# Optimization experiments

Measured on AMD Instinct MI355X. Metric: run time of the kernel, lower is better.

Reference implementation:

```python
import jax, jax.numpy as jnp
import numpy as np

N_ACTIONS = 4
HIDDEN = 32

def setup_inputs() -> dict:
    key = jax.random.key(0)
    ks = jax.random.split(key, 8)
    B, T = 2048, 1024
    prev_actions_onehot = jax.random.uniform(ks[0], (B, T, N_ACTIONS), dtype=jnp.float32)
    prev_rewards = jax.random.normal(ks[1], (B, T, 1), dtype=jnp.float32)
    in_dim = N_ACTIONS + 1
    s_ih = 1.0 / np.sqrt(HIDDEN)
    W_ih = jax.random.uniform(ks[2], (HIDDEN, in_dim), jnp.float32, -s_ih, s_ih)
    W_hh = jax.random.uniform(ks[3], (HIDDEN, HIDDEN), jnp.float32, -s_ih, s_ih)
    b_ih = jax.random.uniform(ks[4], (HIDDEN,), jnp.float32, -s_ih, s_ih)
    b_hh = jax.random.uniform(ks[5], (HIDDEN,), jnp.float32, -s_ih, s_ih)
    W_ro = jax.random.uniform(ks[6], (N_ACTIONS, HIDDEN), jnp.float32, -s_ih, s_ih)
    b_ro = jax.random.uniform(ks[7], (N_ACTIONS,), jnp.float32, -s_ih, s_ih)
    return {
        'prev_actions_onehot': prev_actions_onehot,
        'prev_rewards': prev_rewards,
        'W_ih': W_ih, 'W_hh': W_hh, 'b_ih': b_ih, 'b_hh': b_hh,
        'W_ro': W_ro, 'b_ro': b_ro,
    }

def reference(prev_actions_onehot, prev_rewards, W_ih, W_hh, b_ih, b_hh, W_ro, b_ro):
    # x_seq: [B, T, n_actions+1]
    x_seq = jnp.concatenate([prev_actions_onehot, prev_rewards], axis=-1)
    B = x_seq.shape[0]
    # Precompute the input projection for all steps (parallel): [B, T, H]
    x_proj = jnp.einsum('bti,hi->bth', x_seq, W_ih) + b_ih + b_hh
    h0 = jnp.zeros((B, HIDDEN), dtype=x_seq.dtype)

    def step(h, xp_t):
        # xp_t: [B, H] (already contains x@W_ih^T + b_ih + b_hh)
        h_new = jnp.tanh(xp_t + h @ W_hh.T)
        return h_new, h_new

    # scan over time: move T to leading axis
    h_T, hs = jax.lax.scan(step, h0, jnp.swapaxes(x_proj, 0, 1))
    hs = jnp.swapaxes(hs, 0, 1)  # [B, T, H]
    logits_seq = jnp.einsum('bth,ah->bta', hs, W_ro) + b_ro  # [B, T, n_actions]
    return logits_seq, h_T
```

## Files before the change

### kernel.cpp

```cpp
#include <hip/hip_runtime.h>

#define H 32
#define GPB 8

__device__ __forceinline__ float fast_tanh(float x) {
    float e = __builtin_amdgcn_exp2f(x * 2.8853900817779268f);
    float r = __builtin_amdgcn_rcpf(e + 1.0f);
    return fmaf(-2.0f, r, 1.0f);
}

#define QFMA(acc, p, w, q) \
    asm("v_fmac_f32_dpp %0, %1, %2 quad_perm:[" #q "," #q "," #q "," #q "] row_mask:0xf bank_mask:0xf" \
        : "+v"(acc) : "v"(p), "v"(w))

#define CH8(acc, q) \
    QFMA(acc, pN[0], whh[8*q+0], q); QFMA(acc, pN[1], whh[8*q+1], q); \
    QFMA(acc, pN[2], whh[8*q+2], q); QFMA(acc, pN[3], whh[8*q+3], q); \
    QFMA(acc, pN[4], whh[8*q+4], q); QFMA(acc, pN[5], whh[8*q+5], q); \
    QFMA(acc, pN[6], whh[8*q+6], q); QFMA(acc, pN[7], whh[8*q+7], q)

#define DPPMOV(x, ctrl) \
    __int_as_float(__builtin_amdgcn_update_dpp(0, __float_as_int(x), (ctrl), 0xf, 0xf, true))
#define ROW_SHR1 0x111
#define ROW_SHR2 0x112
#define ROW_SHR4 0x114

__global__ __launch_bounds__(256, 1) void rnn_fused(
    const float* __restrict__ onehot,
    const float* __restrict__ rewards,
    const float* __restrict__ W_ih,
    const float* __restrict__ W_hh,
    const float* __restrict__ b_ih,
    const float* __restrict__ b_hh,
    const float* __restrict__ W_ro,
    const float* __restrict__ b_ro,
    float* __restrict__ out_logits,
    float* __restrict__ out_hT,
    int T)
{
    const int tid = threadIdx.x;
    const int u   = tid & 31;
    const int wl  = tid & 63;
    const int b   = blockIdx.x * GPB + (tid >> 5);
    const int qp  = u & 3;
    const int r   = u >> 3;
    const bool hi = ((u >> 2) & 1) != 0;
    const bool writer = (u & 7) == 7;

    const int ib = ((wl & 32) + 8 * qp) << 2;
    const int idx0 = ib +  0, idx1 = ib +  4, idx2 = ib +  8, idx3 = ib + 12;
    const int idx4 = ib + 16, idx5 = ib + 20, idx6 = ib + 24, idx7 = ib + 28;

    float whh[H];
#pragma unroll
    for (int k = 0; k < 8; ++k) {
        float4 w = *(const float4*)(W_hh + u * H + 4 * k);
        whh[4*k+0] = w.x; whh[4*k+1] = w.y; whh[4*k+2] = w.z; whh[4*k+3] = w.w;
    }
    const float wih0 = W_ih[u*5+0], wih1 = W_ih[u*5+1], wih2 = W_ih[u*5+2],
                wih3 = W_ih[u*5+3], wih4 = W_ih[u*5+4];
    const float bias = b_ih[u] + b_hh[u];
    const float4 wr4 = *(const float4*)(W_ro + r * H + qp * 8 + (hi ? 4 : 0));
    const float bro = b_ro[r];

    const float* oh_ptr = onehot  + (size_t)b * T * 4;
    const float* rw_ptr = rewards + (size_t)b * T;
    float*       lg_ptr = out_logits + (size_t)b * T * 4;

    float4 oh0 = *(const float4*)(oh_ptr + 0);
    float4 oh1 = *(const float4*)(oh_ptr + 4);
    float4 oh2 = *(const float4*)(oh_ptr + 8);
    float4 oh3 = *(const float4*)(oh_ptr + 12);
    float4 rw  = *(const float4*)(rw_ptr);

    float hj = 0.0f;
    float pA[8], pB[8];

    auto readout = [&](const float (&p)[8], int t) {
        float s0 = hi ? p[4] : p[0];
        float s1 = hi ? p[5] : p[1];
        float s2 = hi ? p[6] : p[2];
        float s3 = hi ? p[7] : p[3];
        float s = fmaf(s3, wr4.w, fmaf(s2, wr4.z, fmaf(s1, wr4.y, s0 * wr4.x)));
        s += DPPMOV(s, ROW_SHR1);
        s += DPPMOV(s, ROW_SHR2);
        s += DPPMOV(s, ROW_SHR4);
        if (writer) lg_ptr[(size_t)t * 4 + r] = s + bro;
    };

    auto step = [&](float (&pN)[8], const float (&pO)[8], float xp, int t, bool ro) {
        const int hb = __float_as_int(hj);
        pN[0] = __int_as_float(__builtin_amdgcn_ds_bpermute(idx0, hb));
        pN[1] = __int_as_float(__builtin_amdgcn_ds_bpermute(idx1, hb));
        pN[2] = __int_as_float(__builtin_amdgcn_ds_bpermute(idx2, hb));
        pN[3] = __int_as_float(__builtin_amdgcn_ds_bpermute(idx3, hb));
        pN[4] = __int_as_float(__builtin_amdgcn_ds_bpermute(idx4, hb));
        pN[5] = __int_as_float(__builtin_amdgcn_ds_bpermute(idx5, hb));
        pN[6] = __int_as_float(__builtin_amdgcn_ds_bpermute(idx6, hb));
        pN[7] = __int_as_float(__builtin_amdgcn_ds_bpermute(idx7, hb));
        if (ro) readout(pO, t - 2);
        float a0 = xp, a1 = 0.f, a2 = 0.f, a3 = 0.f;
        CH8(a0, 0);
        CH8(a1, 1);
        CH8(a2, 2);
        CH8(a3, 3);
        hj = fast_tanh((a0 + a1) + (a2 + a3));
    };

#define XP(oh, rwc) fmaf((oh).x, wih0, fmaf((oh).y, wih1, fmaf((oh).z, wih2, \
                     fmaf((oh).w, wih3, fmaf((rwc), wih4, bias)))))

    {
        float xp0 = XP(oh0, rw.x), xp1 = XP(oh1, rw.y),
              xp2 = XP(oh2, rw.z), xp3 = XP(oh3, rw.w);
        oh0 = *(const float4*)(oh_ptr + 16);
        oh1 = *(const float4*)(oh_ptr + 20);
        oh2 = *(const float4*)(oh_ptr + 24);
        oh3 = *(const float4*)(oh_ptr + 28);
        rw  = *(const float4*)(rw_ptr + 4);
        step(pA, pB, xp0, 0, false);
        step(pB, pA, xp1, 1, false);
        step(pA, pB, xp2, 2, true);
        step(pB, pA, xp3, 3, true);
    }

    for (int tb = 4; tb < T; tb += 4) {
        float xp0 = XP(oh0, rw.x), xp1 = XP(oh1, rw.y),
              xp2 = XP(oh2, rw.z), xp3 = XP(oh3, rw.w);
        if (tb + 4 < T) {
            oh0 = *(const float4*)(oh_ptr + (size_t)(tb + 4) * 4);
            oh1 = *(const float4*)(oh_ptr + (size_t)(tb + 5) * 4);
            oh2 = *(const float4*)(oh_ptr + (size_t)(tb + 6) * 4);
            oh3 = *(const float4*)(oh_ptr + (size_t)(tb + 7) * 4);
            rw  = *(const float4*)(rw_ptr + tb + 4);
        }
        step(pA, pB, xp0, tb + 0, true);
        step(pB, pA, xp1, tb + 1, true);
        step(pA, pB, xp2, tb + 2, true);
        step(pB, pA, xp3, tb + 3, true);
    }

    readout(pB, T - 2);
    {
        const int hb = __float_as_int(hj);
        pA[0] = __int_as_float(__builtin_amdgcn_ds_bpermute(idx0, hb));
        pA[1] = __int_as_float(__builtin_amdgcn_ds_bpermute(idx1, hb));
        pA[2] = __int_as_float(__builtin_amdgcn_ds_bpermute(idx2, hb));
        pA[3] = __int_as_float(__builtin_amdgcn_ds_bpermute(idx3, hb));
        pA[4] = __int_as_float(__builtin_amdgcn_ds_bpermute(idx4, hb));
        pA[5] = __int_as_float(__builtin_amdgcn_ds_bpermute(idx5, hb));
        pA[6] = __int_as_float(__builtin_amdgcn_ds_bpermute(idx6, hb));
        pA[7] = __int_as_float(__builtin_amdgcn_ds_bpermute(idx7, hb));
    }
    readout(pA, T - 1);
    out_hT[(size_t)b * H + u] = hj;
}

extern "C" void kernel_launch(void* const* d_in, const int* in_sizes, int n_in,
                              void* d_out, int out_size, void* d_ws, size_t ws_size,
                              hipStream_t stream) {
    const float* onehot  = (const float*)d_in[0];
    const float* rewards = (const float*)d_in[1];
    const float* W_ih    = (const float*)d_in[2];
    const float* W_hh    = (const float*)d_in[3];
    const float* b_ih    = (const float*)d_in[4];
    const float* b_hh    = (const float*)d_in[5];
    const float* W_ro    = (const float*)d_in[6];
    const float* b_ro    = (const float*)d_in[7];

    const int T = 1024;
    const int B = in_sizes[1] / T;

    float* out_logits = (float*)d_out;
    float* out_hT     = (float*)d_out + (size_t)B * T * 4;

    dim3 block(256);
    dim3 grid(B / GPB);
    rnn_fused<<<grid, block, 0, stream>>>(onehot, rewards, W_ih, W_hh,
                                          b_ih, b_hh, W_ro, b_ro,
                                          out_logits, out_hT, T);
}
```

Baseline: 315.2 us.

## Interleave two batch sequences per half-wavefront to hide gather latency

Each 32-lane half-wave now processes two independent batch rows, staggered by half a step. The bpermute gather of one sequence overlaps the matvec of the other, which hides LDS permute latency on the serial recurrence. The upper half of each wavefront exits immediately, so half the lanes go idle. The matvec FMAs are also reordered so the four accumulators interleave. This trades lane utilization for instruction-level parallelism within the dependency chain.

```diff
diff --git a/kernel.cpp b/kernel.cpp
--- a/kernel.cpp
+++ b/kernel.cpp
@@ -1,7 +1,6 @@
 #include <hip/hip_runtime.h>
 
 #define H 32
-#define GPB 8
 
 __device__ __forceinline__ float fast_tanh(float x) {
     float e = __builtin_amdgcn_exp2f(x * 2.8853900817779268f);
@@ -13,17 +12,20 @@
     asm("v_fmac_f32_dpp %0, %1, %2 quad_perm:[" #q "," #q "," #q "," #q "] row_mask:0xf bank_mask:0xf" \
         : "+v"(acc) : "v"(p), "v"(w))
 
-#define CH8(acc, q) \
-    QFMA(acc, pN[0], whh[8*q+0], q); QFMA(acc, pN[1], whh[8*q+1], q); \
-    QFMA(acc, pN[2], whh[8*q+2], q); QFMA(acc, pN[3], whh[8*q+3], q); \
-    QFMA(acc, pN[4], whh[8*q+4], q); QFMA(acc, pN[5], whh[8*q+5], q); \
-    QFMA(acc, pN[6], whh[8*q+6], q); QFMA(acc, pN[7], whh[8*q+7], q)
+#define MV4(i) \
+    QFMA(a0, p[i], whh[i],      0); \
+    QFMA(a1, p[i], whh[8 + i],  1); \
+    QFMA(a2, p[i], whh[16 + i], 2); \
+    QFMA(a3, p[i], whh[24 + i], 3)
 
 #define DPPMOV(x, ctrl) \
     __int_as_float(__builtin_amdgcn_update_dpp(0, __float_as_int(x), (ctrl), 0xf, 0xf, true))
 #define ROW_SHR1 0x111
 #define ROW_SHR2 0x112
 #define ROW_SHR4 0x114
+
+#define XP(oh, rwc) fmaf((oh).x, wih0, fmaf((oh).y, wih1, fmaf((oh).z, wih2, \
+                     fmaf((oh).w, wih3, fmaf((rwc), wih4, bias)))))
 
 __global__ __launch_bounds__(256, 1) void rnn_fused(
     const float* __restrict__ onehot,
@@ -39,15 +41,19 @@
     int T)
 {
     const int tid = threadIdx.x;
+    const int wl  = tid & 63;
+    if (wl >= 32) return;
+
     const int u   = tid & 31;
-    const int wl  = tid & 63;
-    const int b   = blockIdx.x * GPB + (tid >> 5);
+    const int grp = blockIdx.x * 4 + (tid >> 6);
+    const int ba  = grp * 2;
+    const int bb  = ba + 1;
     const int qp  = u & 3;
     const int r   = u >> 3;
     const bool hi = ((u >> 2) & 1) != 0;
     const bool writer = (u & 7) == 7;
 
-    const int ib = ((wl & 32) + 8 * qp) << 2;
+    const int ib = (8 * qp) << 2;
     const int idx0 = ib +  0, idx1 = ib +  4, idx2 = ib +  8, idx3 = ib + 12;
     const int idx4 = ib + 16, idx5 = ib + 20, idx6 = ib + 24, idx7 = ib + 28;
 
@@ -63,20 +69,36 @@
     const float4 wr4 = *(const float4*)(W_ro + r * H + qp * 8 + (hi ? 4 : 0));
     const float bro = b_ro[r];
 
-    const float* oh_ptr = onehot  + (size_t)b * T * 4;
-    const float* rw_ptr = rewards + (size_t)b * T;
-    float*       lg_ptr = out_logits + (size_t)b * T * 4;
-
-    float4 oh0 = *(const float4*)(oh_ptr + 0);
-    float4 oh1 = *(const float4*)(oh_ptr + 4);
-    float4 oh2 = *(const float4*)(oh_ptr + 8);
-    float4 oh3 = *(const float4*)(oh_ptr + 12);
-    float4 rw  = *(const float4*)(rw_ptr);
-
-    float hj = 0.0f;
-    float pA[8], pB[8];
-
-    auto readout = [&](const float (&p)[8], int t) {
+    const float* ohA = onehot  + (size_t)ba * T * 4;
+    const float* rwA = rewards + (size_t)ba * T;
+    float*       lgA = out_logits + (size_t)ba * T * 4;
+    const float* ohB = onehot  + (size_t)bb * T * 4;
+    const float* rwB = rewards + (size_t)bb * T;
+    float*       lgB = out_logits + (size_t)bb * T * 4;
+
+    float4 oA0 = *(const float4*)(ohA + 0), oA1 = *(const float4*)(ohA + 4),
+           oA2 = *(const float4*)(ohA + 8), oA3 = *(const float4*)(ohA + 12);
+    float4 rAv = *(const float4*)(rwA);
+    float4 oB0 = *(const float4*)(ohB + 0), oB1 = *(const float4*)(ohB + 4),
+           oB2 = *(const float4*)(ohB + 8), oB3 = *(const float4*)(ohB + 12);
+    float4 rBv = *(const float4*)(rwB);
+
+    float hA, hB;
+    float pA0[8], pA1[8], pB0[8], pB1[8];
+
+    auto gather = [&](float (&d)[8], float h) {
+        const int hb = __float_as_int(h);
+        d[0] = __int_as_float(__builtin_amdgcn_ds_bpermute(idx0, hb));
+        d[1] = __int_as_float(__builtin_amdgcn_ds_bpermute(idx1, hb));
+        d[2] = __int_as_float(__builtin_amdgcn_ds_bpermute(idx2, hb));
+        d[3] = __int_as_float(__builtin_amdgcn_ds_bpermute(idx3, hb));
+        d[4] = __int_as_float(__builtin_amdgcn_ds_bpermute(idx4, hb));
+        d[5] = __int_as_float(__builtin_amdgcn_ds_bpermute(idx5, hb));
+        d[6] = __int_as_float(__builtin_amdgcn_ds_bpermute(idx6, hb));
+        d[7] = __int_as_float(__builtin_amdgcn_ds_bpermute(idx7, hb));
+    };
+
+    auto readout = [&](const float (&p)[8], float* __restrict__ lg, int t) {
         float s0 = hi ? p[4] : p[0];
         float s1 = hi ? p[5] : p[1];
         float s2 = hi ? p[6] : p[2];
@@ -85,75 +107,75 @@
         s += DPPMOV(s, ROW_SHR1);
         s += DPPMOV(s, ROW_SHR2);
         s += DPPMOV(s, ROW_SHR4);
-        if (writer) lg_ptr[(size_t)t * 4 + r] = s + bro;
-    };
-
-    auto step = [&](float (&pN)[8], const float (&pO)[8], float xp, int t, bool ro) {
-        const int hb = __float_as_int(hj);
-        pN[0] = __int_as_float(__builtin_amdgcn_ds_bpermute(idx0, hb));
-        pN[1] = __int_as_float(__builtin_amdgcn_ds_bpermute(idx1, hb));
-        pN[2] = __int_as_float(__builtin_amdgcn_ds_bpermute(idx2, hb));
-        pN[3] = __int_as_float(__builtin_amdgcn_ds_bpermute(idx3, hb));
-        pN[4] = __int_as_float(__builtin_amdgcn_ds_bpermute(idx4, hb));
-        pN[5] = __int_as_float(__builtin_amdgcn_ds_bpermute(idx5, hb));
-        pN[6] = __int_as_float(__builtin_amdgcn_ds_bpermute(idx6, hb));
-        pN[7] = __int_as_float(__builtin_amdgcn_ds_bpermute(idx7, hb));
-        if (ro) readout(pO, t - 2);
+        if (writer) lg[(size_t)t * 4 + r] = s + bro;
+    };
+
+    auto mv = [&](const float (&p)[8], float xp) -> float {
         float a0 = xp, a1 = 0.f, a2 = 0.f, a3 = 0.f;
-        CH8(a0, 0);
-        CH8(a1, 1);
-        CH8(a2, 2);
-        CH8(a3, 3);
-        hj = fast_tanh((a0 + a1) + (a2 + a3));
-    };
-
-#define XP(oh, rwc) fmaf((oh).x, wih0, fmaf((oh).y, wih1, fmaf((oh).z, wih2, \
-                     fmaf((oh).w, wih3, fmaf((rwc), wih4, bias)))))
+        MV4(0); MV4(1); MV4(2); MV4(3); MV4(4); MV4(5); MV4(6); MV4(7);
+        return fast_tanh((a0 + a1) + (a2 + a3));
+    };
+
+    auto mstep = [&](float (&pAn)[8], const float (&pAo)[8],
+                     float (&pBn)[8], const float (&pBo)[8],
+                     float xpA, float xpB, int t, bool roA, bool roB) {
+        gather(pAn, hA);
+        if (roA) readout(pAo, lgA, t - 2);
+        hB = mv(pBo, xpB);
+        gather(pBn, hB);
+        if (roB) readout(pBo, lgB, t - 1);
+        hA = mv(pAn, xpA);
+    };
 
     {
-        float xp0 = XP(oh0, rw.x), xp1 = XP(oh1, rw.y),
-              xp2 = XP(oh2, rw.z), xp3 = XP(oh3, rw.w);
-        oh0 = *(const float4*)(oh_ptr + 16);
-        oh1 = *(const float4*)(oh_ptr + 20);
-        oh2 = *(const float4*)(oh_ptr + 24);
-        oh3 = *(const float4*)(oh_ptr + 28);
-        rw  = *(const float4*)(rw_ptr + 4);
-        step(pA, pB, xp0, 0, false);
-        step(pB, pA, xp1, 1, false);
-        step(pA, pB, xp2, 2, true);
-        step(pB, pA, xp3, 3, true);
+        float xA0 = XP(oA0, rAv.x), xA1 = XP(oA1, rAv.y),
+              xA2 = XP(oA2, rAv.z), xA3 = XP(oA3, rAv.w);
+        float xB0 = XP(oB0, rBv.x), xB1 = XP(oB1, rBv.y),
+              xB2 = XP(oB2, rBv.z), xB3 = XP(oB3, rBv.w);
+        oA0 = *(const float4*)(ohA + 16); oA1 = *(const float4*)(ohA + 20);
+        oA2 = *(const float4*)(ohA + 24); oA3 = *(const float4*)(ohA + 28);
+        rAv = *(const float4*)(rwA + 4);
+        oB0 = *(const float4*)(ohB + 16); oB1 = *(const float4*)(ohB + 20);
+        oB2 = *(const float4*)(ohB + 24); oB3 = *(const float4*)(ohB + 28);
+        rBv = *(const float4*)(rwB + 4);
+
+        hA = fast_tanh(xA0);
+        hB = fast_tanh(xB0);
+        gather(pB0, hB);
+        mstep(pA1, pA0, pB1, pB0, xA1, xB1, 1, false, true);
+        mstep(pA0, pA1, pB0, pB1, xA2, xB2, 2, true,  true);
+        mstep(pA1, pA0, pB1, pB0, xA3, xB3, 3, true,  true);
     }
 
     for (int tb = 4; tb < T; tb += 4) {
-        float xp0 = XP(oh0, rw.x), xp1 = XP(oh1, rw.y),
-              xp2 = XP(oh2, rw.z), xp3 = XP(oh3, rw.w);
+        float xA0 = XP(oA0, rAv.x), xA1 = XP(oA1, rAv.y),
+              xA2 = XP(oA2, rAv.z), xA3 = XP(oA3, rAv.w);
+        float xB0 = XP(oB0, rBv.x), xB1 = XP(oB1, rBv.y),
+              xB2 = XP(oB2, rBv.z), xB3 = XP(oB3, rBv.w);
         if (tb + 4 < T) {
-            oh0 = *(const float4*)(oh_ptr + (size_t)(tb + 4) * 4);
-            oh1 = *(const float4*)(oh_ptr + (size_t)(tb + 5) * 4);
-            oh2 = *(const float4*)(oh_ptr + (size_t)(tb + 6) * 4);
-            oh3 = *(const float4*)(oh_ptr + (size_t)(tb + 7) * 4);
-            rw  = *(const float4*)(rw_ptr + tb + 4);
+            oA0 = *(const float4*)(ohA + (size_t)(tb + 4) * 4);
+            oA1 = *(const float4*)(ohA + (size_t)(tb + 5) * 4);
+            oA2 = *(const float4*)(ohA + (size_t)(tb + 6) * 4);
+            oA3 = *(const float4*)(ohA + (size_t)(tb + 7) * 4);
+            rAv = *(const float4*)(rwA + tb + 4);
+            oB0 = *(const float4*)(ohB + (size_t)(tb + 4) * 4);
+            oB1 = *(const float4*)(ohB + (size_t)(tb + 5) * 4);
+            oB2 = *(const float4*)(ohB + (size_t)(tb + 6) * 4);
+            oB3 = *(const float4*)(ohB + (size_t)(tb + 7) * 4);
+            rBv = *(const float4*)(rwB + tb + 4);
         }
-        step(pA, pB, xp0, tb + 0, true);
-        step(pB, pA, xp1, tb + 1, true);
-        step(pA, pB, xp2, tb + 2, true);
-        step(pB, pA, xp3, tb + 3, true);
+        mstep(pA0, pA1, pB0, pB1, xA0, xB0, tb + 0, true, true);
+        mstep(pA1, pA0, pB1, pB0, xA1, xB1, tb + 1, true, true);
+        mstep(pA0, pA1, pB0, pB1, xA2, xB2, tb + 2, true, true);
+        mstep(pA1, pA0, pB1, pB0, xA3, xB3, tb + 3, true, true);
     }
 
-    readout(pB, T - 2);
-    {
-        const int hb = __float_as_int(hj);
-        pA[0] = __int_as_float(__builtin_amdgcn_ds_bpermute(idx0, hb));
-        pA[1] = __int_as_float(__builtin_amdgcn_ds_bpermute(idx1, hb));
-        pA[2] = __int_as_float(__builtin_amdgcn_ds_bpermute(idx2, hb));
-        pA[3] = __int_as_float(__builtin_amdgcn_ds_bpermute(idx3, hb));
-        pA[4] = __int_as_float(__builtin_amdgcn_ds_bpermute(idx4, hb));
-        pA[5] = __int_as_float(__builtin_amdgcn_ds_bpermute(idx5, hb));
-        pA[6] = __int_as_float(__builtin_amdgcn_ds_bpermute(idx6, hb));
-        pA[7] = __int_as_float(__builtin_amdgcn_ds_bpermute(idx7, hb));
-    }
-    readout(pA, T - 1);
-    out_hT[(size_t)b * H + u] = hj;
+    readout(pA1, lgA, T - 2);
+    gather(pA0, hA);
+    readout(pB1, lgB, T - 1);
+    readout(pA0, lgA, T - 1);
+    out_hT[(size_t)ba * H + u] = hA;
+    out_hT[(size_t)bb * H + u] = hB;
 }
 
 extern "C" void kernel_launch(void* const* d_in, const int* in_sizes, int n_in,
@@ -175,7 +197,7 @@
     float* out_hT     = (float*)d_out + (size_t)B * T * 4;
 
     dim3 block(256);
-    dim3 grid(B / GPB);
+    dim3 grid(B / 8);
     rnn_fused<<<grid, block, 0, stream>>>(onehot, rewards, W_ih, W_hh,
                                           b_ih, b_hh, W_ro, b_ro,
                                           out_logits, out_hT, T);
```

After: 502.4 us. 1.59x slower.
